# Kernel tuning notes

Measured on AMD Instinct MI355X. Metric: run time of the kernel, lower is better.

The kernel has to match this reference:

```python
import jax, jax.numpy as jnp
import numpy as np

B, N, FD, HD, MD, FS, NM = 8, 64, 128, 256, 64, 80, 6
D = HD + MD  # 320: GNN/decoder operating dim (fixes dim bug in original)
H = W = 128

def _mlp2(x, W1, b1, W2, b2):
    return jax.nn.relu(jax.nn.relu(x @ W1 + b1) @ W2 + b2)

def _forward(object_features, object_attributes, perception_features, object_positions,
             enc_W1, enc_b1, enc_W2, enc_b2, conv1_W, conv1_b, conv2_W, conv2_b,
             edge_W1, edge_b1, edge_W2, edge_b2, gru_Wih, gru_Whh, gru_bih, gru_bhh,
             mode_W1, mode_b1, mode_W2, mode_b2, traj_W1, traj_b1, traj_W2, traj_b2):
    # object encoder: [B,N,FD+8] -> [B,N,HD]
    obj_in = jnp.concatenate([object_features, object_attributes], -1)
    emb = _mlp2(obj_in, enc_W1, enc_b1, enc_W2, enc_b2)
    # map encoder (original discards result via random sampler; kept for faithfulness)
    dn = ('NCHW', 'OIHW', 'NCHW')
    m = jax.nn.relu(jax.lax.conv_general_dilated(perception_features, conv1_W, (1, 1), 'SAME', dimension_numbers=dn) + conv1_b[None, :, None, None])
    m = jax.nn.relu(jax.lax.conv_general_dilated(m, conv2_W, (1, 1), 'SAME', dimension_numbers=dn) + conv2_b[None, :, None, None])
    # sample_map_at_positions returns randn in the original; fixed-seed equivalent
    sampled = jax.random.normal(jax.random.key(42), (B, N, MD), dtype=emb.dtype)
    ctx = jnp.concatenate([emb, sampled], -1)  # [B,N,D]
    # Social GNN, fully vectorized over the ego-node loop i:
    rel = object_positions[:, :, None, :] - object_positions[:, None, :, :]  # [B,N,N,2] = pos[i]-pos[j]
    ego = jnp.broadcast_to(ctx[:, :, None, :], (B, N, N, D))
    nbr = jnp.broadcast_to(ctx[:, None, :, :], (B, N, N, D))
    e = _mlp2(jnp.concatenate([ego, nbr, rel], -1), edge_W1, edge_b1, edge_W2, edge_b2)  # [B,N,N,D]
    mask = (1.0 - jnp.eye(N, dtype=e.dtype))[None, :, :, None]
    agg = (e * mask).sum(2) / (N - 1 + 1e-10)  # [B,N,D]
    # GRUCell(input=concat(ctx,agg), hidden=ctx), torch semantics
    x = jnp.concatenate([ctx, agg], -1)  # [B,N,2D]
    gi = x @ gru_Wih + gru_bih
    gh = ctx @ gru_Whh + gru_bhh
    ir, iz, inn = jnp.split(gi, 3, -1)
    hr, hz, hn = jnp.split(gh, 3, -1)
    r = jax.nn.sigmoid(ir + hr)
    z = jax.nn.sigmoid(iz + hz)
    n = jnp.tanh(inn + r * hn)
    h = (1.0 - z) * n + z * ctx  # [B,N,D]
    # multi-modal trajectory decoder
    mode_probs = jax.nn.softmax(jax.nn.relu(h @ mode_W1 + mode_b1) @ mode_W2 + mode_b2, -1)  # [B,N,NM]
    t = jax.nn.relu(jnp.einsum('bnd,mde->bnme', h, traj_W1) + traj_b1)  # [B,N,NM,D]
    traj = jnp.einsum('bnme,mef->bnmf', t, traj_W2) + traj_b2  # [B,N,NM,FS*2]
    traj = traj.reshape(B, N, NM, FS, 2)
    return traj, mode_probs

def setup_inputs() -> dict:
    key = jax.random.key(0)
    ks = jax.random.split(key, 24)
    p = lambda k, shape: jax.random.normal(k, shape, dtype=jnp.float32) * 0.02
    z = lambda *shape: jnp.zeros(shape, dtype=jnp.float32)
    return {
        'object_features': jax.random.normal(ks[0], (B, N, FD), dtype=jnp.float32),
        'object_attributes': jax.random.normal(ks[1], (B, N, 8), dtype=jnp.float32),
        'perception_features': jax.random.normal(ks[2], (B, 256, H, W), dtype=jnp.float32),
        'object_positions': jax.random.normal(ks[3], (B, N, 2), dtype=jnp.float32),
        'enc_W1': p(ks[4], (FD + 8, HD)), 'enc_b1': z(HD),
        'enc_W2': p(ks[5], (HD, HD)), 'enc_b2': z(HD),
        'conv1_W': p(ks[6], (128, 256, 3, 3)), 'conv1_b': z(128),
        'conv2_W': p(ks[7], (64, 128, 3, 3)), 'conv2_b': z(64),
        'edge_W1': p(ks[8], (2 * D + 2, D)), 'edge_b1': z(D),
        'edge_W2': p(ks[9], (D, D)), 'edge_b2': z(D),
        'gru_Wih': p(ks[10], (2 * D, 3 * D)), 'gru_Whh': p(ks[11], (D, 3 * D)),
        'gru_bih': z(3 * D), 'gru_bhh': z(3 * D),
        'mode_W1': p(ks[12], (D, D)), 'mode_b1': z(D),
        'mode_W2': p(ks[13], (D, NM)), 'mode_b2': z(NM),
        'traj_W1': p(ks[14], (NM, D, D)), 'traj_b1': z(NM, D),
        'traj_W2': p(ks[15], (NM, D, FS * 2)), 'traj_b2': z(NM, FS * 2),
    }

def reference(object_features, object_attributes, perception_features, object_positions,
              enc_W1, enc_b1, enc_W2, enc_b2, conv1_W, conv1_b, conv2_W, conv2_b,
              edge_W1, edge_b1, edge_W2, edge_b2, gru_Wih, gru_Whh, gru_bih, gru_bhh,
              mode_W1, mode_b1, mode_W2, mode_b2, traj_W1, traj_b1, traj_W2, traj_b2):
    return _forward(object_features, object_attributes, perception_features, object_positions,
                    enc_W1, enc_b1, enc_W2, enc_b2, conv1_W, conv1_b, conv2_W, conv2_b,
                    edge_W1, edge_b1, edge_W2, edge_b2, gru_Wih, gru_Whh, gru_bih, gru_bhh,
                    mode_W1, mode_b1, mode_W2, mode_b2, traj_W1, traj_b1, traj_W2, traj_b2)
```

## Files before the change

kernel.cpp:

```cpp
#include <hip/hip_runtime.h>


typedef __attribute__((ext_vector_type(8))) short bf16x8;
typedef __attribute__((ext_vector_type(4))) float f32x4;

__device__ __forceinline__ unsigned short f2bf(float x) {
  unsigned u = __float_as_uint(x);
  return (unsigned short)((u + 0x7fffu + ((u >> 16) & 1u)) >> 16);
}

__device__ __forceinline__ void threefry2x32(unsigned k0, unsigned k1,
                                             unsigned& x0, unsigned& x1) {
  const unsigned ks0 = k0, ks1 = k1, ks2 = k0 ^ k1 ^ 0x1BD11BDAu;
  x0 += ks0; x1 += ks1;
#define TFR(r) { x0 += x1; x1 = (x1 << (r)) | (x1 >> (32 - (r))); x1 ^= x0; }
  TFR(13) TFR(15) TFR(26) TFR(6)  x0 += ks1; x1 += ks2 + 1u;
  TFR(17) TFR(29) TFR(16) TFR(24) x0 += ks2; x1 += ks0 + 2u;
  TFR(13) TFR(15) TFR(26) TFR(6)  x0 += ks0; x1 += ks1 + 3u;
  TFR(17) TFR(29) TFR(16) TFR(24) x0 += ks1; x1 += ks2 + 4u;
  TFR(13) TFR(15) TFR(26) TFR(6)  x0 += ks2; x1 += ks0 + 5u;
#undef TFR
}

__device__ __forceinline__ float erfinv_xla(float x) {
  float w = -logf((1.0f - x) * (1.0f + x));
  float p;
  if (w < 5.0f) {
    w = w - 2.5f;
    p = 2.81022636e-08f;
    p = fmaf(p, w, 3.43273939e-07f);
    p = fmaf(p, w, -3.5233877e-06f);
    p = fmaf(p, w, -4.39150654e-06f);
    p = fmaf(p, w, 0.00021858087f);
    p = fmaf(p, w, -0.00125372503f);
    p = fmaf(p, w, -0.00417768164f);
    p = fmaf(p, w, 0.246640727f);
    p = fmaf(p, w, 1.50140941f);
  } else {
    w = sqrtf(w) - 3.0f;
    p = -0.000200214257f;
    p = fmaf(p, w, 0.000100950558f);
    p = fmaf(p, w, 0.00134934322f);
    p = fmaf(p, w, -0.00367342844f);
    p = fmaf(p, w, 0.00573950773f);
    p = fmaf(p, w, -0.0076224613f);
    p = fmaf(p, w, 0.00943887047f);
    p = fmaf(p, w, 1.00167406f);
    p = fmaf(p, w, 2.83297682f);
  }
  return p * x;
}

__device__ __forceinline__ float jax_normal42(unsigned idx) {
  unsigned x0 = 0u, x1 = idx;
  threefry2x32(0u, 42u, x0, x1);
  unsigned bits = x0 ^ x1;
  float f = __uint_as_float((bits >> 9) | 0x3f800000u) - 1.0f;
  const float lo = -0.99999994f;
  float u = fmaxf(lo, f * 2.0f + lo);
  return 1.41421356237f * erfinv_xla(u);
}

__global__ __launch_bounds__(256)
void k_head(const float* __restrict__ W2e, const float* __restrict__ Wih,
            const float* __restrict__ Whh, const float* __restrict__ T1,
            const float* __restrict__ T2, const float* __restrict__ EW1,
            const float* __restrict__ MW1, const float* __restrict__ MW2,
            unsigned short* __restrict__ ub,
            const float* __restrict__ feat, const float* __restrict__ attr,
            const float* __restrict__ eW1, const float* __restrict__ eb1,
            const float* __restrict__ eW2, const float* __restrict__ eb2,
            float* __restrict__ ctx) {
  __shared__ float s_in[4][136];
  __shared__ float s_h1[4][256];
  const int t = threadIdx.x;

  if (blockIdx.x < 1103) {
    const int id = blockIdx.x * 256 + t;
    if (id >= 282240) return;
    if (id >= 281600) {
      const int rem = id - 281600;
      const int g = rem >> 4, n = rem & 15;
      unsigned short v[8];
#pragma unroll
      for (int e = 0; e < 8; ++e) v[e] = (n < 6) ? f2bf(MW2[(g * 8 + e) * 6 + n]) : 0;
      ushort4* d = (ushort4*)&ub[2252800 + (size_t)rem * 8];
      d[0] = make_ushort4(v[0], v[1], v[2], v[3]);
      d[1] = make_ushort4(v[4], v[5], v[6], v[7]);
      return;
    }
    const float* src;
    unsigned short* dst;
    int rem, N;
    if (id < 12800)       { src = W2e; dst = ub;           rem = id;          N = 320; }
    else if (id < 89600)  { src = Wih; dst = ub + 102400;  rem = id - 12800;  N = 960; }
    else if (id < 128000) { src = Whh; dst = ub + 716800;  rem = id - 89600;  N = 960; }
    else if (id < 204800) { src = T1;  dst = ub + 1024000; rem = id - 128000; N = 320; }
    else if (id < 243200) { src = T2;  dst = ub + 1638400; rem = id - 204800; N = 160; }
    else if (id < 268800) { src = EW1; dst = ub + 1945600; rem = id - 243200; N = 320; }
    else                  { src = MW1; dst = ub + 2150400; rem = id - 268800; N = 320; }
    const int g = rem / N, n = rem - g * N;
    const float* s = src + g * 8 * N + n;
    unsigned short v[8];
#pragma unroll
    for (int e = 0; e < 8; ++e) v[e] = f2bf(s[e * N]);
    ushort4* d = (ushort4*)&dst[(size_t)rem * 8];
    d[0] = make_ushort4(v[0], v[1], v[2], v[3]);
    d[1] = make_ushort4(v[4], v[5], v[6], v[7]);
    return;
  }

  const int r0 = (blockIdx.x - 1103) * 4;
  for (int r = 0; r < 4; ++r) {
    if (t < 128)      s_in[r][t] = feat[(r0 + r) * 128 + t];
    else if (t < 136) s_in[r][t] = attr[(r0 + r) * 8 + (t - 128)];
  }
  __syncthreads();
  float acc[4];
#pragma unroll
  for (int r = 0; r < 4; ++r) acc[r] = eb1[t];
  for (int k = 0; k < 136; ++k) {
    const float w = eW1[k * 256 + t];
#pragma unroll
    for (int r = 0; r < 4; ++r) acc[r] = fmaf(s_in[r][k], w, acc[r]);
  }
#pragma unroll
  for (int r = 0; r < 4; ++r) s_h1[r][t] = fmaxf(acc[r], 0.0f);
  __syncthreads();
#pragma unroll
  for (int r = 0; r < 4; ++r) acc[r] = eb2[t];
  for (int k = 0; k < 256; ++k) {
    const float w = eW2[k * 256 + t];
#pragma unroll
    for (int r = 0; r < 4; ++r) acc[r] = fmaf(s_h1[r][k], w, acc[r]);
  }
#pragma unroll
  for (int r = 0; r < 4; ++r) ctx[(r0 + r) * 320 + t] = fmaxf(acc[r], 0.0f);
  if (t < 64) {
    for (int r = 0; r < 4; ++r)
      ctx[(r0 + r) * 320 + 256 + t] = jax_normal42((unsigned)((r0 + r) * 64 + t));
  }
}

__global__ __launch_bounds__(256)
void k_pqM(const float* __restrict__ ctx, const unsigned short* __restrict__ Bf,
           const float* __restrict__ b1, float* __restrict__ P,
           float* __restrict__ Q) {
  __shared__ __align__(16) unsigned short s_c[40 * 16 * 8];
  const int row0 = blockIdx.x * 16;
  const int half = blockIdx.y;
  const int t = threadIdx.x;
#pragma unroll
  for (int it = 0; it < 3; ++it) {
    const int idx = t + it * 256;
    if (idx < 640) {
      const int row = idx / 40, oct = idx - row * 40;
      const float4 v0 = *(const float4*)&ctx[(row0 + row) * 320 + oct * 8];
      const float4 v1 = *(const float4*)&ctx[(row0 + row) * 320 + oct * 8 + 4];
      ushort4* dst = (ushort4*)&s_c[(oct * 16 + row) * 8];
      dst[0] = make_ushort4(f2bf(v0.x), f2bf(v0.y), f2bf(v0.z), f2bf(v0.w));
      dst[1] = make_ushort4(f2bf(v1.x), f2bf(v1.y), f2bf(v1.z), f2bf(v1.w));
    }
  }
  __syncthreads();

  const int w = t >> 6, l = t & 63, lg = l >> 4, lr = l & 15;
  f32x4 acc[5];
#pragma unroll
  for (int u = 0; u < 5; ++u) acc[u] = (f32x4){0.f, 0.f, 0.f, 0.f};
#pragma unroll
  for (int ks = 0; ks < 10; ++ks) {
    const bf16x8 afr = *(const bf16x8*)&s_c[((ks * 4 + lg) * 16 + lr) * 8];
    bf16x8 bfr[5];
#pragma unroll
    for (int u = 0; u < 5; ++u)
      bfr[u] = *(const bf16x8*)&Bf[(((ks * 4 + lg) * 640) + half * 320 +
                                    w * 80 + u * 16 + lr) * 8];
#pragma unroll
    for (int u = 0; u < 5; ++u)
      acc[u] = __builtin_amdgcn_mfma_f32_16x16x32_bf16(afr, bfr[u], acc[u], 0, 0, 0);
  }
#pragma unroll
  for (int u = 0; u < 5; ++u) {
    const int n = w * 80 + u * 16 + lr;
    const float bias = (half == 0) ? b1[n] : 0.0f;
    float* dst = (half == 0) ? P : Q;
#pragma unroll
    for (int r = 0; r < 4; ++r) {
      const int row = row0 + lg * 4 + r;
      dst[row * 320 + n] = acc[u][r] + bias;
    }
  }
}

__global__ __launch_bounds__(256)
void k_edge(const float* __restrict__ P, const float* __restrict__ Q,
            const float* __restrict__ pos, const float* __restrict__ W1,
            const unsigned short* __restrict__ Bf, const float* __restrict__ b2,
            float* __restrict__ agg) {
  __shared__ __align__(16) unsigned short s_A[40 * 64 * 8];
  const int bx = blockIdx.x;
  const int b = bx >> 6, i = bx & 63;
  const int t = threadIdx.x;
  const int w = t >> 6, l = t & 63;

  {
    const float2 pi = *(const float2*)&pos[b * 128 + 2 * i];
    const float* __restrict__ Prow = P + bx * 320;
    const float* __restrict__ w0 = W1 + 640 * 320;
    const float* __restrict__ w1 = W1 + 641 * 320;
#pragma unroll
    for (int it = 0; it < 10; ++it) {
      const int tau = w * 640 + it * 64 + l;
      const int j = tau / 40;
      const int oct = tau - j * 40;
      const int k0 = oct * 8;
      const float2 pj = *(const float2*)&pos[b * 128 + 2 * j];
      const float rx = pi.x - pj.x, ry = pi.y - pj.y;
      const float* __restrict__ Qrow = Q + (b * 64 + j) * 320;
      const float4 q0 = *(const float4*)&Qrow[k0];
      const float4 q1 = *(const float4*)&Qrow[k0 + 4];
      const float4 p0 = *(const float4*)&Prow[k0];
      const float4 p1 = *(const float4*)&Prow[k0 + 4];
      const float4 a0 = *(const float4*)&w0[k0];
      const float4 a1 = *(const float4*)&w0[k0 + 4];
      const float4 c0 = *(const float4*)&w1[k0];
      const float4 c1 = *(const float4*)&w1[k0 + 4];
      float v[8];
      v[0] = fmaf(ry, c0.x, fmaf(rx, a0.x, p0.x + q0.x));
      v[1] = fmaf(ry, c0.y, fmaf(rx, a0.y, p0.y + q0.y));
      v[2] = fmaf(ry, c0.z, fmaf(rx, a0.z, p0.z + q0.z));
      v[3] = fmaf(ry, c0.w, fmaf(rx, a0.w, p0.w + q0.w));
      v[4] = fmaf(ry, c1.x, fmaf(rx, a1.x, p1.x + q1.x));
      v[5] = fmaf(ry, c1.y, fmaf(rx, a1.y, p1.y + q1.y));
      v[6] = fmaf(ry, c1.z, fmaf(rx, a1.z, p1.z + q1.z));
      v[7] = fmaf(ry, c1.w, fmaf(rx, a1.w, p1.w + q1.w));
      unsigned short u[8];
#pragma unroll
      for (int e = 0; e < 8; ++e) u[e] = f2bf(fmaxf(v[e], 0.0f));
      const int swz = ((oct * 64 + j) * 8) ^ ((oct & 7) << 3);
      *(ushort4*)&s_A[swz]     = make_ushort4(u[0], u[1], u[2], u[3]);
      *(ushort4*)&s_A[swz + 4] = make_ushort4(u[4], u[5], u[6], u[7]);
    }
  }
  __syncthreads();

  f32x4 acc[4][5];
#pragma unroll
  for (int mt = 0; mt < 4; ++mt)
#pragma unroll
    for (int u = 0; u < 5; ++u) acc[mt][u] = (f32x4){0.f, 0.f, 0.f, 0.f};

  const int lg = l >> 4, lr = l & 15;
  const unsigned short* __restrict__ Bbase = Bf + (lg * 320 + w * 80 + lr) * 8;

#pragma unroll 2
  for (int ks = 0; ks < 10; ++ks) {
    const int oct = ks * 4 + lg;
    bf16x8 afr[4];
#pragma unroll
    for (int mt = 0; mt < 4; ++mt) {
      const int elem = ((oct * 64 + mt * 16 + lr) * 8) ^ ((oct & 7) << 3);
      afr[mt] = *(const bf16x8*)&s_A[elem];
    }
    bf16x8 bfr[5];
#pragma unroll
    for (int u = 0; u < 5; ++u)
      bfr[u] = *(const bf16x8*)(Bbase + ks * 10240 + u * 128);
#pragma unroll
    for (int mt = 0; mt < 4; ++mt)
#pragma unroll
      for (int u = 0; u < 5; ++u)
        acc[mt][u] = __builtin_amdgcn_mfma_f32_16x16x32_bf16(
            afr[mt], bfr[u], acc[mt][u], 0, 0, 0);
  }

#pragma unroll
  for (int u = 0; u < 5; ++u) {
    const int n = w * 80 + u * 16 + lr;
    const float bias = b2[n];
    float p = 0.0f;
#pragma unroll
    for (int mt = 0; mt < 4; ++mt) {
#pragma unroll
      for (int r = 0; r < 4; ++r) {
        const int j = mt * 16 + lg * 4 + r;
        const float e = fmaxf(acc[mt][u][r] + bias, 0.0f);
        p += (j != i) ? e : 0.0f;
      }
    }
    p += __shfl_xor(p, 16);
    p += __shfl_xor(p, 32);
    if (l < 16) agg[bx * 320 + n] = p * (1.0f / 63.0f);
  }
}

__global__ __launch_bounds__(256)
void k_gruM(const float* __restrict__ ctx, const float* __restrict__ agg,
            const unsigned short* __restrict__ BfI,
            const unsigned short* __restrict__ BfH,
            const float* __restrict__ bih, const float* __restrict__ bhh,
            float* __restrict__ h) {
  __shared__ __align__(16) unsigned short s_x[80 * 16 * 8];
  const int rb = blockIdx.x / 5, db = blockIdx.x % 5;
  const int row0 = rb * 16, d0 = db * 64;
  const int t = threadIdx.x;

#pragma unroll
  for (int it = 0; it < 5; ++it) {
    const int idx = t + it * 256;
    const int row = idx / 80, oct = idx - row * 80;
    float4 v0, v1;
    if (oct < 40) {
      v0 = *(const float4*)&ctx[(row0 + row) * 320 + oct * 8];
      v1 = *(const float4*)&ctx[(row0 + row) * 320 + oct * 8 + 4];
    } else {
      v0 = *(const float4*)&agg[(row0 + row) * 320 + (oct - 40) * 8];
      v1 = *(const float4*)&agg[(row0 + row) * 320 + (oct - 40) * 8 + 4];
    }
    ushort4* dst = (ushort4*)&s_x[(oct * 16 + row) * 8];
    dst[0] = make_ushort4(f2bf(v0.x), f2bf(v0.y), f2bf(v0.z), f2bf(v0.w));
    dst[1] = make_ushort4(f2bf(v1.x), f2bf(v1.y), f2bf(v1.z), f2bf(v1.w));
  }
  __syncthreads();

  const int w = t >> 6, l = t & 63, lg = l >> 4, lr = l & 15;
  const int d = d0 + w * 16 + lr;

  f32x4 accI[3], accH[3];
#pragma unroll
  for (int g = 0; g < 3; ++g) {
    accI[g] = (f32x4){0.f, 0.f, 0.f, 0.f};
    accH[g] = (f32x4){0.f, 0.f, 0.f, 0.f};
  }

#pragma unroll 2
  for (int ks = 0; ks < 20; ++ks) {
    const bf16x8 afr = *(const bf16x8*)&s_x[((ks * 4 + lg) * 16 + lr) * 8];
    bf16x8 bfr[3];
#pragma unroll
    for (int g = 0; g < 3; ++g)
      bfr[g] = *(const bf16x8*)&BfI[((ks * 4 + lg) * 960 + g * 320 + d) * 8];
#pragma unroll
    for (int g = 0; g < 3; ++g)
      accI[g] = __builtin_amdgcn_mfma_f32_16x16x32_bf16(afr, bfr[g], accI[g], 0, 0, 0);
  }
#pragma unroll 2
  for (int ks = 0; ks < 10; ++ks) {
    const bf16x8 afr = *(const bf16x8*)&s_x[((ks * 4 + lg) * 16 + lr) * 8];
    bf16x8 bfr[3];
#pragma unroll
    for (int g = 0; g < 3; ++g)
      bfr[g] = *(const bf16x8*)&BfH[((ks * 4 + lg) * 960 + g * 320 + d) * 8];
#pragma unroll
    for (int g = 0; g < 3; ++g)
      accH[g] = __builtin_amdgcn_mfma_f32_16x16x32_bf16(afr, bfr[g], accH[g], 0, 0, 0);
  }

  const float b_ir = bih[d], b_iz = bih[320 + d], b_in = bih[640 + d];
  const float b_hr = bhh[d], b_hz = bhh[320 + d], b_hn = bhh[640 + d];
#pragma unroll
  for (int r = 0; r < 4; ++r) {
    const int row = row0 + lg * 4 + r;
    const float ir = accI[0][r] + b_ir;
    const float iz = accI[1][r] + b_iz;
    const float inn = accI[2][r] + b_in;
    const float hr = accH[0][r] + b_hr;
    const float hz = accH[1][r] + b_hz;
    const float hn = accH[2][r] + b_hn;
    const float rr = 1.0f / (1.0f + expf(-(ir + hr)));
    const float zz = 1.0f / (1.0f + expf(-(iz + hz)));
    const float nn = tanhf(fmaf(rr, hn, inn));
    const float c = ctx[row * 320 + d];
    h[row * 320 + d] = (1.0f - zz) * nn + zz * c;
  }
}

__global__ __launch_bounds__(256)
void k_tail(const float* __restrict__ h, const unsigned short* __restrict__ MB1,
            const float* __restrict__ mb1, const unsigned short* __restrict__ MB2,
            const float* __restrict__ mb2, const unsigned short* __restrict__ TB1,
            const float* __restrict__ tb1, const unsigned short* __restrict__ TB2,
            const float* __restrict__ tb2, float* __restrict__ out) {
  __shared__ __align__(16) unsigned short s_buf[20480];
  __shared__ float s_l[32][6];
  const int t = threadIdx.x;
  const int w = t >> 6, l = t & 63, lg = l >> 4, lr = l & 15;

  if (blockIdx.x < 16) {
    unsigned short* s_h = s_buf;
    unsigned short* s_t = s_buf + 10240;
    const int row0 = blockIdx.x * 32;
#pragma unroll
    for (int it = 0; it < 5; ++it) {
      const int idx = t + it * 256;
      const int row = idx / 40, oct = idx - row * 40;
      const float4 v0 = *(const float4*)&h[(row0 + row) * 320 + oct * 8];
      const float4 v1 = *(const float4*)&h[(row0 + row) * 320 + oct * 8 + 4];
      ushort4* dst = (ushort4*)&s_h[(oct * 32 + row) * 8];
      dst[0] = make_ushort4(f2bf(v0.x), f2bf(v0.y), f2bf(v0.z), f2bf(v0.w));
      dst[1] = make_ushort4(f2bf(v1.x), f2bf(v1.y), f2bf(v1.z), f2bf(v1.w));
    }
    __syncthreads();

    f32x4 acc1[2][5];
#pragma unroll
    for (int mt = 0; mt < 2; ++mt)
#pragma unroll
      for (int u = 0; u < 5; ++u) acc1[mt][u] = (f32x4){0.f, 0.f, 0.f, 0.f};
#pragma unroll
    for (int ks = 0; ks < 10; ++ks) {
      bf16x8 afr[2];
#pragma unroll
      for (int mt = 0; mt < 2; ++mt)
        afr[mt] = *(const bf16x8*)&s_h[(((ks * 4 + lg) * 32) + mt * 16 + lr) * 8];
      bf16x8 bfr[5];
#pragma unroll
      for (int u = 0; u < 5; ++u)
        bfr[u] = *(const bf16x8*)&MB1[((ks * 4 + lg) * 320 + w * 80 + u * 16 + lr) * 8];
#pragma unroll
      for (int mt = 0; mt < 2; ++mt)
#pragma unroll
        for (int u = 0; u < 5; ++u)
          acc1[mt][u] = __builtin_amdgcn_mfma_f32_16x16x32_bf16(
              afr[mt], bfr[u], acc1[mt][u], 0, 0, 0);
    }
#pragma unroll
    for (int u = 0; u < 5; ++u) {
      const int n = w * 80 + u * 16 + lr;
      const float bias = mb1[n];
#pragma unroll
      for (int mt = 0; mt < 2; ++mt) {
#pragma unroll
        for (int r = 0; r < 4; ++r) {
          const int row = mt * 16 + lg * 4 + r;
          s_t[((n >> 3) * 32 + row) * 8 + (n & 7)] =
              f2bf(fmaxf(acc1[mt][u][r] + bias, 0.0f));
        }
      }
    }
    __syncthreads();

    if (w < 2) {
      f32x4 acc2 = (f32x4){0.f, 0.f, 0.f, 0.f};
#pragma unroll
      for (int ks = 0; ks < 10; ++ks) {
        const bf16x8 afr = *(const bf16x8*)&s_t[(((ks * 4 + lg) * 32) + w * 16 + lr) * 8];
        const bf16x8 bfr = *(const bf16x8*)&MB2[((ks * 4 + lg) * 16 + lr) * 8];
        acc2 = __builtin_amdgcn_mfma_f32_16x16x32_bf16(afr, bfr, acc2, 0, 0, 0);
      }
      if (lr < 6) {
#pragma unroll
        for (int r = 0; r < 4; ++r)
          s_l[w * 16 + lg * 4 + r][lr] = acc2[r] + mb2[lr];
      }
    }
    __syncthreads();

    if (t < 32) {
      float v[6];
#pragma unroll
      for (int q = 0; q < 6; ++q) v[q] = s_l[t][q];
      float mx = v[0];
#pragma unroll
      for (int q = 1; q < 6; ++q) mx = fmaxf(mx, v[q]);
      float sum = 0.0f;
#pragma unroll
      for (int q = 0; q < 6; ++q) { v[q] = expf(v[q] - mx); sum += v[q]; }
      const float inv = 1.0f / sum;
#pragma unroll
      for (int q = 0; q < 6; ++q) out[491520 + (row0 + t) * 6 + q] = v[q] * inv;
    }
    return;
  }

  const int idx0 = blockIdx.x - 16;
  const int m = idx0 >> 5, rb = idx0 & 31;
  unsigned short* s_h = s_buf;
  unsigned short* s_t = s_buf + 5120;
  const int row0 = rb * 16;

#pragma unroll
  for (int it = 0; it < 3; ++it) {
    const int idx = t + it * 256;
    if (idx < 640) {
      const int row = idx / 40, oct = idx - row * 40;
      const float4 v0 = *(const float4*)&h[(row0 + row) * 320 + oct * 8];
      const float4 v1 = *(const float4*)&h[(row0 + row) * 320 + oct * 8 + 4];
      ushort4* dst = (ushort4*)&s_h[(oct * 16 + row) * 8];
      dst[0] = make_ushort4(f2bf(v0.x), f2bf(v0.y), f2bf(v0.z), f2bf(v0.w));
      dst[1] = make_ushort4(f2bf(v1.x), f2bf(v1.y), f2bf(v1.z), f2bf(v1.w));
    }
  }
  __syncthreads();

  f32x4 acc1[5];
#pragma unroll
  for (int u = 0; u < 5; ++u) acc1[u] = (f32x4){0.f, 0.f, 0.f, 0.f};
  const unsigned short* __restrict__ B1m = TB1 + m * 102400;
#pragma unroll
  for (int ks = 0; ks < 10; ++ks) {
    const bf16x8 afr = *(const bf16x8*)&s_h[((ks * 4 + lg) * 16 + lr) * 8];
    bf16x8 bfr[5];
#pragma unroll
    for (int u = 0; u < 5; ++u)
      bfr[u] = *(const bf16x8*)&B1m[((ks * 4 + lg) * 320 + w * 80 + u * 16 + lr) * 8];
#pragma unroll
    for (int u = 0; u < 5; ++u)
      acc1[u] = __builtin_amdgcn_mfma_f32_16x16x32_bf16(afr, bfr[u], acc1[u], 0, 0, 0);
  }
#pragma unroll
  for (int u = 0; u < 5; ++u) {
    const int n = w * 80 + u * 16 + lr;
    const float bias = tb1[m * 320 + n];
#pragma unroll
    for (int r = 0; r < 4; ++r) {
      const int row = lg * 4 + r;
      s_t[((n >> 3) * 16 + row) * 8 + (n & 7)] =
          f2bf(fmaxf(acc1[u][r] + bias, 0.0f));
    }
  }
  __syncthreads();

  const int nb = (w == 0) ? 0 : (w == 1) ? 3 : (w == 2) ? 6 : 7;
  f32x4 acc2[3];
#pragma unroll
  for (int u = 0; u < 3; ++u) acc2[u] = (f32x4){0.f, 0.f, 0.f, 0.f};
  const unsigned short* __restrict__ B2m = TB2 + m * 51200;
#pragma unroll
  for (int ks = 0; ks < 10; ++ks) {
    const bf16x8 afr = *(const bf16x8*)&s_t[((ks * 4 + lg) * 16 + lr) * 8];
    bf16x8 bfr[3];
#pragma unroll
    for (int u = 0; u < 3; ++u)
      bfr[u] = *(const bf16x8*)&B2m[((ks * 4 + lg) * 160 + (nb + u) * 16 + lr) * 8];
#pragma unroll
    for (int u = 0; u < 3; ++u)
      acc2[u] = __builtin_amdgcn_mfma_f32_16x16x32_bf16(afr, bfr[u], acc2[u], 0, 0, 0);
  }
#pragma unroll
  for (int u = 0; u < 3; ++u) {
    const int n = (nb + u) * 16 + lr;
    const float bias = tb2[m * 160 + n];
#pragma unroll
    for (int r = 0; r < 4; ++r) {
      const int row = row0 + lg * 4 + r;
      out[(row * 6 + m) * 160 + n] = acc2[u][r] + bias;
    }
  }
}

extern "C" void kernel_launch(void* const* d_in, const int* in_sizes, int n_in,
                              void* d_out, int out_size, void* d_ws, size_t ws_size,
                              hipStream_t stream) {
  (void)in_sizes; (void)n_in; (void)out_size; (void)ws_size;
  const float* feat  = (const float*)d_in[0];
  const float* attr  = (const float*)d_in[1];
  const float* pos   = (const float*)d_in[3];
  const float* encW1 = (const float*)d_in[4];
  const float* encb1 = (const float*)d_in[5];
  const float* encW2 = (const float*)d_in[6];
  const float* encb2 = (const float*)d_in[7];
  const float* edgW1 = (const float*)d_in[12];
  const float* edgb1 = (const float*)d_in[13];
  const float* edgW2 = (const float*)d_in[14];
  const float* edgb2 = (const float*)d_in[15];
  const float* Wih   = (const float*)d_in[16];
  const float* Whh   = (const float*)d_in[17];
  const float* bih   = (const float*)d_in[18];
  const float* bhh   = (const float*)d_in[19];
  const float* mW1   = (const float*)d_in[20];
  const float* mb1   = (const float*)d_in[21];
  const float* mW2   = (const float*)d_in[22];
  const float* mb2   = (const float*)d_in[23];
  const float* tW1   = (const float*)d_in[24];
  const float* tb1   = (const float*)d_in[25];
  const float* tW2   = (const float*)d_in[26];
  const float* tb2   = (const float*)d_in[27];

  float* out = (float*)d_out;
  float* ws  = (float*)d_ws;
  float* ctx  = ws;
  float* P    = ws + 163840;
  float* Q    = ws + 327680;
  float* agg  = ws + 491520;
  float* hbuf = ws + 655360;
  unsigned short* ub = (unsigned short*)(ws + 819200);
  unsigned short* W2bf  = ub;
  unsigned short* WihBf = ub + 102400;
  unsigned short* WhhBf = ub + 716800;
  unsigned short* T1bf  = ub + 1024000;
  unsigned short* T2bf  = ub + 1638400;
  unsigned short* EW1bf = ub + 1945600;
  unsigned short* MW1bf = ub + 2150400;
  unsigned short* MW2bf = ub + 2252800;

  k_head<<<1231, 256, 0, stream>>>(edgW2, Wih, Whh, tW1, tW2, edgW1, mW1, mW2, ub,
                                   feat, attr, encW1, encb1, encW2, encb2, ctx);
  k_pqM<<<dim3(32, 2), 256, 0, stream>>>(ctx, EW1bf, edgb1, P, Q);
  k_edge<<<512, 256, 0, stream>>>(P, Q, pos, edgW1, W2bf, edgb2, agg);
  k_gruM<<<160, 256, 0, stream>>>(ctx, agg, WihBf, WhhBf, bih, bhh, hbuf);
  k_tail<<<208, 256, 0, stream>>>(hbuf, MW1bf, mb1, MW2bf, mb2,
                                  T1bf, tb1, T2bf, tb2, out);
}
```

Before: 78.35 us.

## Spread weight bf16 conversions across kernels just ahead of their consumers

Weight fp32-to-bf16 conversion used to run entirely in the first kernel. It is now split so each kernel converts only the weights needed by a later kernel, in extra blocks that run alongside that kernel's own compute. The goal is to shorten the critical first kernel and hide conversion work under the pq and edge kernels. The cost is larger grids in later kernels and extra branch code.

```diff
diff --git a/kernel.cpp b/kernel.cpp
--- a/kernel.cpp
+++ b/kernel.cpp
@@ -61,56 +61,38 @@
   return 1.41421356237f * erfinv_xla(u);
 }
 
+__device__ __forceinline__ void cvt_octet(const float* __restrict__ src,
+                                          unsigned short* __restrict__ dst,
+                                          int rem, int N) {
+  const int g = rem / N, n = rem - g * N;
+  const float* s = src + g * 8 * N + n;
+  unsigned short v[8];
+#pragma unroll
+  for (int e = 0; e < 8; ++e) v[e] = f2bf(s[e * N]);
+  ushort4* d = (ushort4*)&dst[(size_t)rem * 8];
+  d[0] = make_ushort4(v[0], v[1], v[2], v[3]);
+  d[1] = make_ushort4(v[4], v[5], v[6], v[7]);
+}
+
 __global__ __launch_bounds__(256)
-void k_head(const float* __restrict__ W2e, const float* __restrict__ Wih,
-            const float* __restrict__ Whh, const float* __restrict__ T1,
-            const float* __restrict__ T2, const float* __restrict__ EW1,
-            const float* __restrict__ MW1, const float* __restrict__ MW2,
-            unsigned short* __restrict__ ub,
-            const float* __restrict__ feat, const float* __restrict__ attr,
+void k_head(const float* __restrict__ feat, const float* __restrict__ attr,
             const float* __restrict__ eW1, const float* __restrict__ eb1,
             const float* __restrict__ eW2, const float* __restrict__ eb2,
-            float* __restrict__ ctx) {
+            float* __restrict__ ctx,
+            const float* __restrict__ W2e, const float* __restrict__ EW1,
+            unsigned short* __restrict__ ub) {
   __shared__ float s_in[4][136];
   __shared__ float s_h1[4][256];
   const int t = threadIdx.x;
 
-  if (blockIdx.x < 1103) {
-    const int id = blockIdx.x * 256 + t;
-    if (id >= 282240) return;
-    if (id >= 281600) {
-      const int rem = id - 281600;
-      const int g = rem >> 4, n = rem & 15;
-      unsigned short v[8];
-#pragma unroll
-      for (int e = 0; e < 8; ++e) v[e] = (n < 6) ? f2bf(MW2[(g * 8 + e) * 6 + n]) : 0;
-      ushort4* d = (ushort4*)&ub[2252800 + (size_t)rem * 8];
-      d[0] = make_ushort4(v[0], v[1], v[2], v[3]);
-      d[1] = make_ushort4(v[4], v[5], v[6], v[7]);
-      return;
-    }
-    const float* src;
-    unsigned short* dst;
-    int rem, N;
-    if (id < 12800)       { src = W2e; dst = ub;           rem = id;          N = 320; }
-    else if (id < 89600)  { src = Wih; dst = ub + 102400;  rem = id - 12800;  N = 960; }
-    else if (id < 128000) { src = Whh; dst = ub + 716800;  rem = id - 89600;  N = 960; }
-    else if (id < 204800) { src = T1;  dst = ub + 1024000; rem = id - 128000; N = 320; }
-    else if (id < 243200) { src = T2;  dst = ub + 1638400; rem = id - 204800; N = 160; }
-    else if (id < 268800) { src = EW1; dst = ub + 1945600; rem = id - 243200; N = 320; }
-    else                  { src = MW1; dst = ub + 2150400; rem = id - 268800; N = 320; }
-    const int g = rem / N, n = rem - g * N;
-    const float* s = src + g * 8 * N + n;
-    unsigned short v[8];
-#pragma unroll
-    for (int e = 0; e < 8; ++e) v[e] = f2bf(s[e * N]);
-    ushort4* d = (ushort4*)&dst[(size_t)rem * 8];
-    d[0] = make_ushort4(v[0], v[1], v[2], v[3]);
-    d[1] = make_ushort4(v[4], v[5], v[6], v[7]);
+  if (blockIdx.x >= 128) {
+    const int id = (blockIdx.x - 128) * 256 + t;
+    if (id < 12800)      cvt_octet(W2e, ub, id, 320);
+    else if (id < 38400) cvt_octet(EW1, ub + 1945600, id - 12800, 320);
     return;
   }
 
-  const int r0 = (blockIdx.x - 1103) * 4;
+  const int r0 = blockIdx.x * 4;
   for (int r = 0; r < 4; ++r) {
     if (t < 128)      s_in[r][t] = feat[(r0 + r) * 128 + t];
     else if (t < 136) s_in[r][t] = attr[(r0 + r) * 8 + (t - 128)];
@@ -145,11 +127,20 @@
 __global__ __launch_bounds__(256)
 void k_pqM(const float* __restrict__ ctx, const unsigned short* __restrict__ Bf,
            const float* __restrict__ b1, float* __restrict__ P,
-           float* __restrict__ Q) {
+           float* __restrict__ Q, const float* __restrict__ Wih,
+           const float* __restrict__ Whh, unsigned short* __restrict__ ub) {
   __shared__ __align__(16) unsigned short s_c[40 * 16 * 8];
-  const int row0 = blockIdx.x * 16;
-  const int half = blockIdx.y;
   const int t = threadIdx.x;
+
+  if (blockIdx.x >= 64) {
+    const int id = (blockIdx.x - 64) * 256 + t;
+    if (id < 76800)       cvt_octet(Wih, ub + 102400, id, 960);
+    else if (id < 115200) cvt_octet(Whh, ub + 716800, id - 76800, 960);
+    return;
+  }
+
+  const int row0 = (blockIdx.x >> 1) * 16;
+  const int half = blockIdx.x & 1;
 #pragma unroll
   for (int it = 0; it < 3; ++it) {
     const int idx = t + it * 256;
@@ -197,11 +188,35 @@
 void k_edge(const float* __restrict__ P, const float* __restrict__ Q,
             const float* __restrict__ pos, const float* __restrict__ W1,
             const unsigned short* __restrict__ Bf, const float* __restrict__ b2,
-            float* __restrict__ agg) {
+            float* __restrict__ agg,
+            const float* __restrict__ T1, const float* __restrict__ T2,
+            const float* __restrict__ MW1, const float* __restrict__ MW2,
+            unsigned short* __restrict__ ub) {
   __shared__ __align__(16) unsigned short s_A[40 * 64 * 8];
+  const int t = threadIdx.x;
+
+  if (blockIdx.x >= 512) {
+    const int id = (blockIdx.x - 512) * 256 + t;
+    if (id >= 128640) return;
+    if (id >= 128000) {
+      const int rem = id - 128000;
+      const int g = rem >> 4, n = rem & 15;
+      unsigned short v[8];
+#pragma unroll
+      for (int e = 0; e < 8; ++e) v[e] = (n < 6) ? f2bf(MW2[(g * 8 + e) * 6 + n]) : 0;
+      ushort4* d = (ushort4*)&ub[2252800 + (size_t)rem * 8];
+      d[0] = make_ushort4(v[0], v[1], v[2], v[3]);
+      d[1] = make_ushort4(v[4], v[5], v[6], v[7]);
+      return;
+    }
+    if (id < 76800)       cvt_octet(T1, ub + 1024000, id, 320);
+    else if (id < 115200) cvt_octet(T2, ub + 1638400, id - 76800, 160);
+    else                  cvt_octet(MW1, ub + 2150400, id - 115200, 320);
+    return;
+  }
+
   const int bx = blockIdx.x;
   const int b = bx >> 6, i = bx & 63;
-  const int t = threadIdx.x;
   const int w = t >> 6, l = t & 63;
 
   {
@@ -595,10 +610,11 @@
   unsigned short* MW1bf = ub + 2150400;
   unsigned short* MW2bf = ub + 2252800;
 
-  k_head<<<1231, 256, 0, stream>>>(edgW2, Wih, Whh, tW1, tW2, edgW1, mW1, mW2, ub,
-                                   feat, attr, encW1, encb1, encW2, encb2, ctx);
-  k_pqM<<<dim3(32, 2), 256, 0, stream>>>(ctx, EW1bf, edgb1, P, Q);
-  k_edge<<<512, 256, 0, stream>>>(P, Q, pos, edgW1, W2bf, edgb2, agg);
+  k_head<<<278, 256, 0, stream>>>(feat, attr, encW1, encb1, encW2, encb2, ctx,
+                                  edgW2, edgW1, ub);
+  k_pqM<<<514, 256, 0, stream>>>(ctx, EW1bf, edgb1, P, Q, Wih, Whh, ub);
+  k_edge<<<1015, 256, 0, stream>>>(P, Q, pos, edgW1, W2bf, edgb2, agg,
+                                   tW1, tW2, mW1, mW2, ub);
   k_gruM<<<160, 256, 0, stream>>>(ctx, agg, WihBf, WhhBf, bih, bhh, hbuf);
   k_tail<<<208, 256, 0, stream>>>(hbuf, MW1bf, mb1, MW2bf, mb2,
                                   T1bf, tb1, T2bf, tb2, out);
```

Result: no change. 78.82 us (+0.6%).
